# Kernel optimization log

Hardware: AMD Instinct MI355X
Metric: run time of the kernel (lower is better)

The kernel has to match this reference:

```python
import jax, jax.numpy as jnp
import numpy as np

B, N, C_IN, H, C_OUT = 8, 1024, 256, 4, 256
C = C_OUT // H  # per-head dim = 64
ALPHA = 0.2
NEG_INF = -9e15


def setup_inputs() -> dict:
    key = jax.random.key(0)
    k1, k2, k3, k4, k5 = jax.random.split(key, 5)
    node_feats = jax.random.normal(k1, (B, N, C_IN), dtype=jnp.float32)
    adj_matrix = jax.random.randint(k2, (B, N, N), 0, 2, dtype=jnp.int32)
    # include self-loops as GAT expects
    eye = jnp.eye(N, dtype=jnp.int32)[None]
    adj_matrix = jnp.maximum(adj_matrix, eye)
    # xavier_uniform with gain=1.414
    def xavier(k, shape, fan_in, fan_out, gain=1.414):
        lim = gain * np.sqrt(6.0 / (fan_in + fan_out))
        return jax.random.uniform(k, shape, jnp.float32, -lim, lim)
    W = xavier(k3, (C_OUT, C_IN), C_IN, C_OUT)          # projection weight [out,in]
    b = jnp.zeros((C_OUT,), dtype=jnp.float32)           # projection bias
    a = xavier(k4, (H, 2 * C), 2 * C, H)                 # attention vector per head
    return {"node_feats": node_feats, "adj_matrix": adj_matrix, "W": W, "b": b, "a": a}


def reference(node_feats, adj_matrix, W, b, a):
    Bb, Nn, _ = node_feats.shape
    Hh, twoC = a.shape
    Cc = twoC // 2
    # linear projection -> [B, N, H, C]
    h = (node_feats @ W.T + b).reshape(Bb, Nn, Hh, Cc)
    # edge logit(i,j) = leakyrelu(a . [h_i, h_j]) = leakyrelu(a1.h_i + a2.h_j)
    a_src, a_dst = a[:, :Cc], a[:, Cc:]
    l_src = jnp.einsum('bihc,hc->bih', h, a_src)  # [B,N,H]
    l_dst = jnp.einsum('bjhc,hc->bjh', h, a_dst)  # [B,N,H]
    logits = jax.nn.leaky_relu(l_src[:, :, None, :] + l_dst[:, None, :, :], ALPHA)  # [B,N,N,H]
    logits = jnp.where(adj_matrix[..., None] == 1, logits, NEG_INF)
    probs = jax.nn.softmax(logits, axis=2)  # softmax over neighbors j
    out = jnp.einsum('bijh,bjhc->bihc', probs, h)  # aggregate
    return out.reshape(Bb, Nn, Hh * Cc)  # concat heads
```

## Files before the change

### kernel.cpp

```cpp
#include <hip/hip_runtime.h>
#include <hip/hip_bf16.h>

#define BN   8
#define NN   1024
#define CIN  256
#define COUT 256
#define HH   4
#define CC   64
#define ALPHA_C 0.2f
#define LOG2E_C 1.4426950408889634f

#if __has_builtin(__builtin_amdgcn_exp2f)
#define EXP2F(x) __builtin_amdgcn_exp2f(x)
#else
#define EXP2F(x) exp2f(x)
#endif

typedef __attribute__((ext_vector_type(8))) short short8;
typedef __attribute__((ext_vector_type(4))) float f32x4;

__device__ __forceinline__ unsigned short f2bf(float x) {
    __hip_bfloat16 h = __float2bfloat16(x);
    return *(unsigned short*)&h;
}
__device__ __forceinline__ float bf2f(unsigned short u) {
    return __uint_as_float(((unsigned int)u) << 16);
}
__device__ __forceinline__ void gl_lds16(const void* g, void* l) {
    __builtin_amdgcn_global_load_lds(
        (const __attribute__((address_space(1))) void*)g,
        (__attribute__((address_space(3))) void*)l, 16, 0, 0);
}

__global__ __launch_bounds__(256) void kw_pack(
    const float* __restrict__ W, unsigned short* __restrict__ Whp, unsigned short* __restrict__ Wlp)
{
    const int bid = blockIdx.x;
    const int n = threadIdx.x;
    const int fi = n * 64 + (bid >> 2) * 8 + (bid & 3) * 2;
    const float4* W4 = (const float4*)W;
    float4 wa = W4[fi], wb = W4[fi + 1];
    float xs[8] = {wa.x, wa.y, wa.z, wa.w, wb.x, wb.y, wb.z, wb.w};
    unsigned short hh[8], ll[8];
    #pragma unroll
    for (int e = 0; e < 8; ++e) {
        hh[e] = f2bf(xs[e]);
        ll[e] = f2bf(xs[e] - bf2f(hh[e]));
    }
    *(uint4*)(Whp + ((size_t)bid * 256 + n) * 8) = *(uint4*)hh;
    *(uint4*)(Wlp + ((size_t)bid * 256 + n) * 8) = *(uint4*)ll;
}

__global__ __launch_bounds__(1024, 1) void k1_gemm(
    const float* __restrict__ X, const float* __restrict__ bias, const float* __restrict__ a,
    const int* __restrict__ adj, const unsigned short* __restrict__ Whp,
    const unsigned short* __restrict__ Wlp, unsigned short* __restrict__ hbf_p,
    float* __restrict__ lsrc_t, float* __restrict__ ldst_t, unsigned int* __restrict__ bmG)
{
    __shared__ __align__(16) unsigned short Xh[32 * 256];
    __shared__ __align__(16) unsigned short Xl[32 * 256];
    __shared__ float lsP[2][8][2][16];

    const int bid = blockIdx.x;
    const int b  = bid & 7;
    const int tj = bid >> 3;
    const int row0 = b * NN + tj * 32;
    const int tid = threadIdx.x;
    const int wv = tid >> 6, l = tid & 63, il = l & 15, jg = l >> 4;
    const int mq = wv >> 3, no = wv & 7;

    {
        #pragma unroll
        for (int rr = 0; rr < 2; ++rr) {
            const int r = 2 * wv + rr;
            const int* ap = adj + ((size_t)(row0 + r)) * NN;
            int av[16];
            #pragma unroll
            for (int it = 0; it < 16; ++it) av[it] = ap[it * 64 + l];
            #pragma unroll
            for (int it = 0; it < 16; ++it) {
                unsigned long long mb = __ballot(av[it] != 0);
                if (l == 0) {
                    bmG[((size_t)(row0 + r)) * 32 + 2 * it    ] = (unsigned int)mb;
                    bmG[((size_t)(row0 + r)) * 32 + 2 * it + 1] = (unsigned int)(mb >> 32);
                }
            }
        }
    }

    {
        const float4* X4 = (const float4*)(X + (size_t)row0 * CIN);
        #pragma unroll
        for (int it = 0; it < 2; ++it) {
            int f = it * 1024 + tid;
            int r = f >> 6, k4 = f & 63;
            float4 x = X4[f];
            unsigned short h0 = f2bf(x.x), h1 = f2bf(x.y), h2 = f2bf(x.z), h3 = f2bf(x.w);
            unsigned short l0 = f2bf(x.x - bf2f(h0)), l1 = f2bf(x.y - bf2f(h1));
            unsigned short l2 = f2bf(x.z - bf2f(h2)), l3 = f2bf(x.w - bf2f(h3));
            unsigned short hs[4] = {h0, h1, h2, h3}, ls[4] = {l0, l1, l2, l3};
            int off = r * 512 + ((k4 * 8) ^ ((r & 7) << 4));
            *(uint2*)((char*)Xh + off) = *(uint2*)hs;
            *(uint2*)((char*)Xl + off) = *(uint2*)ls;
        }
    }
    __syncthreads();

    f32x4 acc0 = {0.f, 0.f, 0.f, 0.f}, acc1 = acc0;
    {
        const int abase = (mq * 16 + il) * 512;
        const int swz = (il & 7) << 4;
        const short8* Wh8 = (const short8*)Whp;
        const short8* Wl8 = (const short8*)Wlp;
        const int nb = no * 32 + il;
        #pragma unroll
        for (int kc = 0; kc < 8; ++kc) {
            const int ab = abase + ((kc * 64 + jg * 16) ^ swz);
            short8 Ah = *(const short8*)((const char*)Xh + ab);
            short8 Al = *(const short8*)((const char*)Xl + ab);
            const int pidx = (kc * 4 + jg) * 256 + nb;
            short8 Bh0 = Wh8[pidx],      Bl0 = Wl8[pidx];
            short8 Bh1 = Wh8[pidx + 16], Bl1 = Wl8[pidx + 16];
            acc0 = __builtin_amdgcn_mfma_f32_16x16x32_bf16(Ah, Bh0, acc0, 0, 0, 0);
            acc1 = __builtin_amdgcn_mfma_f32_16x16x32_bf16(Ah, Bh1, acc1, 0, 0, 0);
            acc0 = __builtin_amdgcn_mfma_f32_16x16x32_bf16(Ah, Bl0, acc0, 0, 0, 0);
            acc1 = __builtin_amdgcn_mfma_f32_16x16x32_bf16(Ah, Bl1, acc1, 0, 0, 0);
            acc0 = __builtin_amdgcn_mfma_f32_16x16x32_bf16(Al, Bh0, acc0, 0, 0, 0);
            acc1 = __builtin_amdgcn_mfma_f32_16x16x32_bf16(Al, Bh1, acc1, 0, 0, 0);
        }
    }

    const int c0 = no * 32 + il, c1 = c0 + 16;
    const float bia0 = bias[c0], bia1 = bias[c1];
    const int hh = no >> 1;
    const int cc0 = c0 & 63, cc1 = c1 & 63;
    const float as0 = a[hh * 128 + cc0],      as1 = a[hh * 128 + cc1];
    const float ad0 = a[hh * 128 + 64 + cc0], ad1 = a[hh * 128 + 64 + cc1];

    float v0[4], v1[4], psrc[4], pdst[4];
    #pragma unroll
    for (int r = 0; r < 4; ++r) {
        v0[r] = acc0[r] + bia0;
        v1[r] = acc1[r] + bia1;
        psrc[r] = v0[r] * as0 + v1[r] * as1;
        pdst[r] = v0[r] * ad0 + v1[r] * ad1;
    }
    #pragma unroll
    for (int off = 8; off >= 1; off >>= 1) {
        #pragma unroll
        for (int r = 0; r < 4; ++r) {
            psrc[r] += __shfl_xor(psrc[r], off);
            pdst[r] += __shfl_xor(pdst[r], off);
        }
    }
    __syncthreads();

    unsigned short* hp = Xh;
    #pragma unroll
    for (int r = 0; r < 4; ++r) {
        int m = mq * 16 + 4 * jg + r;
        int base = (m >> 3) * 128 + (m & 7);
        hp[(c0 >> 6) * 2048 + ((c0 & 63) >> 4) * 512 + base + (c0 & 15) * 8] = f2bf(v0[r]);
        hp[(c1 >> 6) * 2048 + ((c1 & 63) >> 4) * 512 + base + (c1 & 15) * 8] = f2bf(v1[r]);
    }
    if (il == 0) {
        #pragma unroll
        for (int r = 0; r < 4; ++r) {
            lsP[0][no][mq][4 * jg + r] = psrc[r];
            lsP[1][no][mq][4 * jg + r] = pdst[r];
        }
    }
    __syncthreads();

    {
        uint4* dst4 = (uint4*)(hbf_p + (size_t)(b * 32 + tj) * 8192);
        dst4[tid] = ((const uint4*)hp)[tid];
    }
    if (tid < 256) {
        int sd = tid >> 7, rem = tid & 127, h2 = rem >> 5, m = rem & 31;
        float v = lsP[sd][2 * h2][m >> 4][m & 15] + lsP[sd][2 * h2 + 1][m >> 4][m & 15];
        float* dst = sd ? ldst_t : lsrc_t;
        dst[((size_t)b * HH + h2) * NN + tj * 32 + m] = v;
    }
}

__global__ __launch_bounds__(1024, 1) void k2_attn(
    const unsigned short* __restrict__ hbf_p, const unsigned int* __restrict__ bmG,
    const float* __restrict__ lsrc_t, const float* __restrict__ ldst_t,
    float* __restrict__ out)
{
    __shared__ __align__(16) char smem[151808];
    __shared__ float lsumS[4][4][32];

    unsigned short* hS  = (unsigned short*)smem;
    unsigned int*  bmS  = (unsigned int*)(smem + 131072);
    float*        ldstS = (float*)(smem + 147712);

    const int bid = blockIdx.x;
    const int b  = bid & 7;
    const int h  = (bid >> 3) & 3;
    const int i0 = (bid >> 5) * 128;
    const int tid = threadIdx.x;
    const int wv = tid >> 6, l = tid & 63, il = l & 15, jg = l >> 4;
    const int rg = wv >> 2, jq = wv & 3;

    {
        #pragma unroll
        for (int k = 0; k < 2; ++k) {
            const int tj = wv * 2 + k;
            #pragma unroll
            for (int cs = 0; cs < 4; ++cs) {
                gl_lds16(hbf_p + ((((size_t)(b * 32 + tj)) * 1024 + h * 256 + cs * 64 + l) << 3),
                         hS + (size_t)(tj * 256 + cs * 64 + l) * 8);
            }
        }
    }
    {
        const unsigned int* bsrc = bmG + ((size_t)(b * NN + i0)) * 32;
        #pragma unroll
        for (int k = 0; k < 4; ++k) {
            int idx = k * 1024 + tid;
            int r = idx >> 5, w = idx & 31;
            bmS[w * 130 + r] = bsrc[idx];
        }
    }
    if (tid < 256) {
        float4 v = ((const float4*)(ldst_t + ((size_t)(b * HH + h)) * NN))[tid];
        v.x *= LOG2E_C; v.y *= LOG2E_C; v.z *= LOG2E_C; v.w *= LOG2E_C;
        ((float4*)ldstS)[tid] = v;
    }

    const float* lsrc_b = lsrc_t + ((size_t)(b * HH + h)) * NN + i0 + rg * 32;
    const float lsv0 = lsrc_b[il] * LOG2E_C;
    const float lsv1 = lsrc_b[16 + il] * LOG2E_C;

    __syncthreads();

    float mx = -3.4e38f;
    #pragma unroll
    for (int jt = 0; jt < 16; ++jt) mx = fmaxf(mx, ldstS[jt * 64 + l]);
    #pragma unroll
    for (int off = 32; off >= 1; off >>= 1) mx = fmaxf(mx, __shfl_xor(mx, off));
    float mr0, mr1;
    { float t_ = lsv0 + mx; mr0 = fmaxf(t_, ALPHA_C * t_); }
    { float t_ = lsv1 + mx; mr1 = fmaxf(t_, ALPHA_C * t_); }

    f32x4 z4 = {0.f,0.f,0.f,0.f};
    f32x4 a00 = z4, a01 = z4, a02 = z4, a03 = z4;
    f32x4 a10 = z4, a11 = z4, a12 = z4, a13 = z4;
    f32x4 s0 = z4, s1 = z4;
    const short8 ones8 = {0x3F80, 0x3F80, 0x3F80, 0x3F80, 0x3F80, 0x3F80, 0x3F80, 0x3F80};

    const short8* hS8 = (const short8*)hS;

    #pragma unroll
    for (int t = 0; t < 8; ++t) {
        const int tj = jq * 8 + t;
        short8 c0 = hS8[tj * 256 +   0 + l];
        short8 c1 = hS8[tj * 256 +  64 + l];
        short8 c2 = hS8[tj * 256 + 128 + l];
        short8 c3 = hS8[tj * 256 + 192 + l];
        const unsigned int bw0 = bmS[tj * 130 + rg * 32 + il] >> (jg * 8);
        const unsigned int bw1 = bmS[tj * 130 + rg * 32 + 16 + il] >> (jg * 8);
        const float4 dA = *(const float4*)(ldstS + tj * 32 + jg * 8);
        const float4 dB = *(const float4*)(ldstS + tj * 32 + jg * 8 + 4);

        short8 af0, af1;
        #define PELEM(AF, E, DV, BWV, LSV, MR) {                         \
            float t_ = (LSV) + (DV);                                     \
            float u_ = fmaxf(t_, ALPHA_C * t_);                          \
            float e_ = EXP2F(u_ - (MR));                                 \
            int m_ = ((int)((BWV) << (31 - (E)))) >> 31;                 \
            AF[E] = (short)((__float_as_uint(e_) >> 16) & (unsigned)m_); }
        PELEM(af0, 0, dA.x, bw0, lsv0, mr0)
        PELEM(af0, 1, dA.y, bw0, lsv0, mr0)
        PELEM(af0, 2, dA.z, bw0, lsv0, mr0)
        PELEM(af0, 3, dA.w, bw0, lsv0, mr0)
        PELEM(af0, 4, dB.x, bw0, lsv0, mr0)
        PELEM(af0, 5, dB.y, bw0, lsv0, mr0)
        PELEM(af0, 6, dB.z, bw0, lsv0, mr0)
        PELEM(af0, 7, dB.w, bw0, lsv0, mr0)
        PELEM(af1, 0, dA.x, bw1, lsv1, mr1)
        PELEM(af1, 1, dA.y, bw1, lsv1, mr1)
        PELEM(af1, 2, dA.z, bw1, lsv1, mr1)
        PELEM(af1, 3, dA.w, bw1, lsv1, mr1)
        PELEM(af1, 4, dB.x, bw1, lsv1, mr1)
        PELEM(af1, 5, dB.y, bw1, lsv1, mr1)
        PELEM(af1, 6, dB.z, bw1, lsv1, mr1)
        PELEM(af1, 7, dB.w, bw1, lsv1, mr1)
        #undef PELEM

        a00 = __builtin_amdgcn_mfma_f32_16x16x32_bf16(af0, c0, a00, 0, 0, 0);
        a01 = __builtin_amdgcn_mfma_f32_16x16x32_bf16(af0, c1, a01, 0, 0, 0);
        a02 = __builtin_amdgcn_mfma_f32_16x16x32_bf16(af0, c2, a02, 0, 0, 0);
        a03 = __builtin_amdgcn_mfma_f32_16x16x32_bf16(af0, c3, a03, 0, 0, 0);
        s0  = __builtin_amdgcn_mfma_f32_16x16x32_bf16(af0, ones8, s0, 0, 0, 0);
        a10 = __builtin_amdgcn_mfma_f32_16x16x32_bf16(af1, c0, a10, 0, 0, 0);
        a11 = __builtin_amdgcn_mfma_f32_16x16x32_bf16(af1, c1, a11, 0, 0, 0);
        a12 = __builtin_amdgcn_mfma_f32_16x16x32_bf16(af1, c2, a12, 0, 0, 0);
        a13 = __builtin_amdgcn_mfma_f32_16x16x32_bf16(af1, c3, a13, 0, 0, 0);
        s1  = __builtin_amdgcn_mfma_f32_16x16x32_bf16(af1, ones8, s1, 0, 0, 0);
    }

    if (il == 0) {
        #pragma unroll
        for (int r = 0; r < 4; ++r) {
            lsumS[jq][rg][4 * jg + r]      = s0[r];
            lsumS[jq][rg][16 + 4 * jg + r] = s1[r];
        }
    }
    __syncthreads();

    float* red0 = (float*)smem;
    float* red1 = red0 + 128 * 68;
    {
        float* rb = (jq & 1) ? red1 : red0;
        const int rbase = rg * 32 + 4 * jg;
        #define STROW(ACC, ROFF, CS, OP) {                                   \
            rb[(rbase + (ROFF) + 0) * 68 + (CS) * 16 + il] OP ACC[0];        \
            rb[(rbase + (ROFF) + 1) * 68 + (CS) * 16 + il] OP ACC[1];        \
            rb[(rbase + (ROFF) + 2) * 68 + (CS) * 16 + il] OP ACC[2];        \
            rb[(rbase + (ROFF) + 3) * 68 + (CS) * 16 + il] OP ACC[3]; }
        #define STOREALL(OP) {                                               \
            STROW(a00, 0, 0, OP) STROW(a01, 0, 1, OP)                        \
            STROW(a02, 0, 2, OP) STROW(a03, 0, 3, OP)                        \
            STROW(a10, 16, 0, OP) STROW(a11, 16, 1, OP)                      \
            STROW(a12, 16, 2, OP) STROW(a13, 16, 3, OP) }
        if (jq < 2) STOREALL(=)
        __syncthreads();
        if (jq >= 2) STOREALL(+=)
        __syncthreads();
        #undef STROW
        #undef STOREALL
    }

    #pragma unroll
    for (int pass = 0; pass < 2; ++pass) {
        int row = pass * 64 + (tid >> 4);
        int c4  = tid & 15;
        float4 v0 = *(const float4*)(red0 + row * 68 + c4 * 4);
        float4 v1 = *(const float4*)(red1 + row * 68 + c4 * 4);
        float ls = lsumS[0][row >> 5][row & 31] + lsumS[1][row >> 5][row & 31]
                 + lsumS[2][row >> 5][row & 31] + lsumS[3][row >> 5][row & 31];
        float inv = 1.0f / ls;
        float4 o = make_float4((v0.x + v1.x) * inv, (v0.y + v1.y) * inv,
                               (v0.z + v1.z) * inv, (v0.w + v1.w) * inv);
        *(float4*)(out + ((size_t)(b * NN + i0 + row)) * COUT + h * 64 + c4 * 4) = o;
    }
}

extern "C" void kernel_launch(void* const* d_in, const int* in_sizes, int n_in,
                              void* d_out, int out_size, void* d_ws, size_t ws_size,
                              hipStream_t stream) {
    const float* X    = (const float*)d_in[0];
    const int*   adj  = (const int*)  d_in[1];
    const float* W    = (const float*)d_in[2];
    const float* bias = (const float*)d_in[3];
    const float* a    = (const float*)d_in[4];
    float* out = (float*)d_out;

    unsigned short* hbf_p = (unsigned short*)d_ws;
    float* lsrc_t = (float*)(hbf_p + (size_t)BN * 32 * 8192);
    float* ldst_t = lsrc_t + (size_t)BN * HH * NN;
    unsigned short* Whp = (unsigned short*)(ldst_t + (size_t)BN * HH * NN);
    unsigned short* Wlp = Whp + 65536;
    unsigned int*   bmG = (unsigned int*)(Wlp + 65536);

    kw_pack<<<32, 256, 0, stream>>>(W, Whp, Wlp);
    k1_gemm<<<256, 1024, 0, stream>>>(X, bias, a, adj, Whp, Wlp, hbf_p, lsrc_t, ldst_t, bmG);
    k2_attn<<<256, 1024, 0, stream>>>(hbf_p, bmG, lsrc_t, ldst_t, out);
}
```

Baseline: 43.28 us.

## Move adjacency bitmask construction into widened prep kernel with W packing

```diff
diff --git a/kernel.cpp b/kernel.cpp
--- a/kernel.cpp
+++ b/kernel.cpp
@@ -10,12 +10,6 @@
 #define ALPHA_C 0.2f
 #define LOG2E_C 1.4426950408889634f
 
-#if __has_builtin(__builtin_amdgcn_exp2f)
-#define EXP2F(x) __builtin_amdgcn_exp2f(x)
-#else
-#define EXP2F(x) exp2f(x)
-#endif
-
 typedef __attribute__((ext_vector_type(8))) short short8;
 typedef __attribute__((ext_vector_type(4))) float f32x4;
 
@@ -32,30 +26,50 @@
         (__attribute__((address_space(3))) void*)l, 16, 0, 0);
 }
 
-__global__ __launch_bounds__(256) void kw_pack(
-    const float* __restrict__ W, unsigned short* __restrict__ Whp, unsigned short* __restrict__ Wlp)
+__global__ __launch_bounds__(256) void kprep(
+    const float* __restrict__ W, const int* __restrict__ adj,
+    unsigned short* __restrict__ Whp, unsigned short* __restrict__ Wlp,
+    unsigned int* __restrict__ bmG)
 {
-    const int bid = blockIdx.x;
-    const int n = threadIdx.x;
-    const int fi = n * 64 + (bid >> 2) * 8 + (bid & 3) * 2;
-    const float4* W4 = (const float4*)W;
-    float4 wa = W4[fi], wb = W4[fi + 1];
-    float xs[8] = {wa.x, wa.y, wa.z, wa.w, wb.x, wb.y, wb.z, wb.w};
-    unsigned short hh[8], ll[8];
-    #pragma unroll
-    for (int e = 0; e < 8; ++e) {
-        hh[e] = f2bf(xs[e]);
-        ll[e] = f2bf(xs[e] - bf2f(hh[e]));
-    }
-    *(uint4*)(Whp + ((size_t)bid * 256 + n) * 8) = *(uint4*)hh;
-    *(uint4*)(Wlp + ((size_t)bid * 256 + n) * 8) = *(uint4*)ll;
+    if (blockIdx.x < 2048) {
+        const int bid = blockIdx.x;
+        const int b  = bid & 7;
+        const int rl = bid >> 3;
+        const int wv = threadIdx.x >> 6;
+        const int l  = threadIdx.x & 63;
+        const int row = b * NN + rl * 4 + wv;
+        const int* arow = adj + (size_t)row * NN;
+        #pragma unroll 4
+        for (int it = 0; it < 16; ++it) {
+            int av = arow[it * 64 + l];
+            unsigned long long mb = __ballot(av != 0);
+            if (l == 0) {
+                bmG[row * 32 + 2 * it    ] = (unsigned int)mb;
+                bmG[row * 32 + 2 * it + 1] = (unsigned int)(mb >> 32);
+            }
+        }
+    } else {
+        const int bid = blockIdx.x - 2048;
+        const int n = threadIdx.x;
+        const int fi = n * 64 + (bid >> 2) * 8 + (bid & 3) * 2;
+        const float4* W4 = (const float4*)W;
+        float4 wa = W4[fi], wb = W4[fi + 1];
+        float xs[8] = {wa.x, wa.y, wa.z, wa.w, wb.x, wb.y, wb.z, wb.w};
+        unsigned short hh[8], ll[8];
+        #pragma unroll
+        for (int e = 0; e < 8; ++e) {
+            hh[e] = f2bf(xs[e]);
+            ll[e] = f2bf(xs[e] - bf2f(hh[e]));
+        }
+        *(uint4*)(Whp + ((size_t)bid * 256 + n) * 8) = *(uint4*)hh;
+        *(uint4*)(Wlp + ((size_t)bid * 256 + n) * 8) = *(uint4*)ll;
+    }
 }
 
 __global__ __launch_bounds__(1024, 1) void k1_gemm(
     const float* __restrict__ X, const float* __restrict__ bias, const float* __restrict__ a,
-    const int* __restrict__ adj, const unsigned short* __restrict__ Whp,
-    const unsigned short* __restrict__ Wlp, unsigned short* __restrict__ hbf_p,
-    float* __restrict__ lsrc_t, float* __restrict__ ldst_t, unsigned int* __restrict__ bmG)
+    const unsigned short* __restrict__ Whp, const unsigned short* __restrict__ Wlp,
+    unsigned short* __restrict__ hbf_p, float* __restrict__ lsrc_t, float* __restrict__ ldst_t)
 {
     __shared__ __align__(16) unsigned short Xh[32 * 256];
     __shared__ __align__(16) unsigned short Xl[32 * 256];
@@ -68,25 +82,6 @@
     const int tid = threadIdx.x;
     const int wv = tid >> 6, l = tid & 63, il = l & 15, jg = l >> 4;
     const int mq = wv >> 3, no = wv & 7;
-
-    {
-        #pragma unroll
-        for (int rr = 0; rr < 2; ++rr) {
-            const int r = 2 * wv + rr;
-            const int* ap = adj + ((size_t)(row0 + r)) * NN;
-            int av[16];
-            #pragma unroll
-            for (int it = 0; it < 16; ++it) av[it] = ap[it * 64 + l];
-            #pragma unroll
-            for (int it = 0; it < 16; ++it) {
-                unsigned long long mb = __ballot(av[it] != 0);
-                if (l == 0) {
-                    bmG[((size_t)(row0 + r)) * 32 + 2 * it    ] = (unsigned int)mb;
-                    bmG[((size_t)(row0 + r)) * 32 + 2 * it + 1] = (unsigned int)(mb >> 32);
-                }
-            }
-        }
-    }
 
     {
         const float4* X4 = (const float4*)(X + (size_t)row0 * CIN);
@@ -269,7 +264,7 @@
         #define PELEM(AF, E, DV, BWV, LSV, MR) {                         \
             float t_ = (LSV) + (DV);                                     \
             float u_ = fmaxf(t_, ALPHA_C * t_);                          \
-            float e_ = EXP2F(u_ - (MR));                                 \
+            float e_ = exp2f(u_ - (MR));                                 \
             int m_ = ((int)((BWV) << (31 - (E)))) >> 31;                 \
             AF[E] = (short)((__float_as_uint(e_) >> 16) & (unsigned)m_); }
         PELEM(af0, 0, dA.x, bw0, lsv0, mr0)
@@ -366,7 +361,7 @@
     unsigned short* Wlp = Whp + 65536;
     unsigned int*   bmG = (unsigned int*)(Wlp + 65536);
 
-    kw_pack<<<32, 256, 0, stream>>>(W, Whp, Wlp);
-    k1_gemm<<<256, 1024, 0, stream>>>(X, bias, a, adj, Whp, Wlp, hbf_p, lsrc_t, ldst_t, bmG);
+    kprep<<<2048 + 32, 256, 0, stream>>>(W, adj, Whp, Wlp, bmG);
+    k1_gemm<<<256, 1024, 0, stream>>>(X, bias, a, Whp, Wlp, hbf_p, lsrc_t, ldst_t);
     k2_attn<<<256, 1024, 0, stream>>>(hbf_p, bmG, lsrc_t, ldst_t, out);
 }
```

After: 44.70 us. 3.3% more time.
